# Performance work log

Measured on AMD Instinct MI355X. Metric: run time of the kernel, lower is better.

The kernel has to match this reference:

```python
import jax, jax.numpy as jnp
import numpy as np

DECAY = 0.8
EPS = 1e-05
COMMIT_W = 0.25
N, D, K = 32768, 128, 4096


def setup_inputs() -> dict:
    key = jax.random.key(0)
    k1, k2, k3, k4 = jax.random.split(key, 4)
    x = jax.random.normal(k1, (N, D), dtype=jnp.float32)
    embed = jax.random.normal(k2, (1, K, D), dtype=jnp.float32)
    cluster_size = jax.random.uniform(k3, (1, K), dtype=jnp.float32)
    embed_avg = jax.random.normal(k4, (1, K, D), dtype=jnp.float32)
    return {"x": x, "embed": embed, "cluster_size": cluster_size, "embed_avg": embed_avg}


def reference(x, embed, cluster_size, embed_avg):
    # x: [n, d]; embed: [1, K, d] (num_codebooks = 1, squeezed as in batched_embedding)
    e = embed[0]                                   # [K, d]
    K_ = e.shape[0]
    # negative squared euclidean distance (== -cdist^2 ordering, same argmin as -cdist)
    x2 = jnp.sum(x * x, axis=-1, keepdims=True)    # [n, 1]
    e2 = jnp.sum(e * e, axis=-1)                   # [K]
    dist = -(x2 - 2.0 * (x @ e.T) + e2)            # [n, K]
    embed_ind = jnp.argmax(dist, axis=-1)          # [n] cluster assignment (argmin distance)
    # differentiable embedding lookup (one-hot @ embed == gather)
    quantize = jnp.take(e, embed_ind, axis=0)      # [n, d]
    # EMA codebook statistics (training-time buffer updates)
    ones = jnp.ones((x.shape[0],), dtype=x.dtype)
    bins = jax.ops.segment_sum(ones, embed_ind, num_segments=K_)         # [K] bincount
    embed_sum = jax.ops.segment_sum(x, embed_ind, num_segments=K_)       # [K, d] scatter-add
    cs_new = cluster_size[0] * DECAY + (1.0 - DECAY) * bins
    ea_new = embed_avg[0] * DECAY + (1.0 - DECAY) * embed_sum
    n_total = jnp.sum(cs_new)
    cluster = (cs_new + EPS) / (n_total + K_ * EPS) * n_total            # laplace smoothing
    embed_normalized = ea_new / cluster[:, None]                         # [K, d]
    # commitment loss: mse(quantize.detach(), x) * weight
    commit_loss = COMMIT_W * jnp.mean((jax.lax.stop_gradient(quantize) - x) ** 2)
    return (quantize, embed_ind, commit_loss, cs_new[None], embed_normalized[None])
```

## Files before the change

kernel.cpp:

```cpp
#include <hip/hip_runtime.h>

#define NROWS 32768
#define DIM   128
#define KCODES 4096
#define DECAYF 0.8f
#define EPSF 1e-5f
#define COMMITW 0.25f

typedef _Float16 half8 __attribute__((ext_vector_type(8)));
typedef _Float16 half2v __attribute__((ext_vector_type(2)));
typedef float float4v __attribute__((ext_vector_type(4)));

__global__ __launch_bounds__(256) void esplit_kernel(const float* __restrict__ embed,
                                                     _Float16* __restrict__ estg,
                                                     float* __restrict__ e2h) {
    int code = blockIdx.x * 4 + (threadIdx.x >> 6);
    int lane = threadIdx.x & 63;
    float2 v = ((const float2*)(embed + (size_t)code * DIM))[lane];
    float s = v.x * v.x + v.y * v.y;
    #pragma unroll
    for (int off = 32; off > 0; off >>= 1) s += __shfl_down(s, off, 64);
    if (lane == 0) e2h[code] = 0.5f * s;

    int d = lane * 2;
    int ks = d >> 5, q = (d >> 3) & 3, j = d & 7;
    _Float16 h0 = (_Float16)v.x, l0 = (_Float16)(v.x - (float)h0);
    _Float16 h1 = (_Float16)v.y, l1 = (_Float16)(v.y - (float)h1);
    int chunk = code >> 6, c6 = code & 63;
    size_t base = (size_t)chunk * 16384;
    size_t hidx = base + (size_t)(( 0 + ks * 4 + q) * 64 + c6) * 8 + j;
    size_t lidx = base + (size_t)((16 + ks * 4 + q) * 64 + c6) * 8 + j;
    *(half2v*)&estg[hidx] = (half2v){h0, h1};
    *(half2v*)&estg[lidx] = (half2v){l0, l1};
}

__global__ __launch_bounds__(512, 2) void argmax_kernel(const float* __restrict__ x,
                                                        const _Float16* __restrict__ estg,
                                                        const float* __restrict__ e2h,
                                                        int* __restrict__ ind,
                                                        float* __restrict__ out_ind,
                                                        int* __restrict__ bins,
                                                        float* __restrict__ loss) {
    __shared__ float rv[8][64];
    __shared__ int   ri[8][64];
    __shared__ float x2s[128];

    int tid = threadIdx.x;
    int lane = tid & 63;
    int w = tid >> 6;
    int j = w & 3;
    int rh = w >> 2;
    int m15 = lane & 15;
    int q = (lane >> 4) & 3;
    int n0 = blockIdx.x * 128;

    half8 Ah[4][4], Al[4][4];
    float xsq[4];
    #pragma unroll
    for (int rt = 0; rt < 4; ++rt) {
        xsq[rt] = 0.f;
        #pragma unroll
        for (int ks = 0; ks < 4; ++ks) {
            const float* p = x + (size_t)(n0 + rh * 64 + rt * 16 + m15) * DIM + ks * 32 + q * 8;
            float4 a = *(const float4*)p;
            float4 b = *(const float4*)(p + 4);
            float f[8] = {a.x, a.y, a.z, a.w, b.x, b.y, b.z, b.w};
            half8 H, L;
            #pragma unroll
            for (int e = 0; e < 8; ++e) {
                _Float16 h = (_Float16)f[e];
                H[e] = h;
                L[e] = (_Float16)(f[e] - (float)h);
                xsq[rt] += f[e] * f[e];
            }
            Ah[rt][ks] = H;
            Al[rt][ks] = L;
        }
        xsq[rt] += __shfl_xor(xsq[rt], 16, 64);
        xsq[rt] += __shfl_xor(xsq[rt], 32, 64);
    }
    if (j == 0 && lane < 16) {
        #pragma unroll
        for (int rt = 0; rt < 4; ++rt) x2s[rh * 64 + rt * 16 + m15] = xsq[rt];
    }

    float best[4][4];
    int   bidx[4][4];
    #pragma unroll
    for (int rt = 0; rt < 4; ++rt)
        #pragma unroll
        for (int r = 0; r < 4; ++r) { best[rt][r] = -3.0e38f; bidx[rt][r] = 0; }

    const _Float16* bbase = estg + (size_t)(j * 16 + m15) * 8 + (size_t)q * 512;
    const int cm = j * 16 + m15;

    half8 B0h[4], B0l[4], B1h[4], B1l[4];
    float e20, e21;

    {
        const _Float16* cb = bbase;
        #pragma unroll
        for (int ks = 0; ks < 4; ++ks) {
            B0h[ks] = *(const half8*)(cb + ks * 2048);
            B0l[ks] = *(const half8*)(cb + 8192 + ks * 2048);
        }
        e20 = e2h[cm];
    }

    #pragma unroll 1
    for (int ch = 0; ch < 64; ch += 2) {
        {
            const _Float16* cb = bbase + (size_t)(ch + 1) * 16384;
            #pragma unroll
            for (int ks = 0; ks < 4; ++ks) {
                B1h[ks] = *(const half8*)(cb + ks * 2048);
                B1l[ks] = *(const half8*)(cb + 8192 + ks * 2048);
            }
            e21 = e2h[(ch + 1) * 64 + cm];
        }
        {
            float4v acc[4];
            #pragma unroll
            for (int rt = 0; rt < 4; ++rt) acc[rt] = (float4v){-e20, -e20, -e20, -e20};
            #pragma unroll
            for (int ks = 0; ks < 4; ++ks)
                #pragma unroll
                for (int rt = 0; rt < 4; ++rt) {
                    acc[rt] = __builtin_amdgcn_mfma_f32_16x16x32_f16(Ah[rt][ks], B0h[ks], acc[rt], 0, 0, 0);
                    acc[rt] = __builtin_amdgcn_mfma_f32_16x16x32_f16(Al[rt][ks], B0h[ks], acc[rt], 0, 0, 0);
                    acc[rt] = __builtin_amdgcn_mfma_f32_16x16x32_f16(Ah[rt][ks], B0l[ks], acc[rt], 0, 0, 0);
                }
            int c = ch * 64 + cm;
            #pragma unroll
            for (int rt = 0; rt < 4; ++rt)
                #pragma unroll
                for (int r = 0; r < 4; ++r) {
                    float s = acc[rt][r];
                    if (s > best[rt][r]) { best[rt][r] = s; bidx[rt][r] = c; }
                }
        }
        if (ch + 2 < 64) {
            const _Float16* cb = bbase + (size_t)(ch + 2) * 16384;
            #pragma unroll
            for (int ks = 0; ks < 4; ++ks) {
                B0h[ks] = *(const half8*)(cb + ks * 2048);
                B0l[ks] = *(const half8*)(cb + 8192 + ks * 2048);
            }
            e20 = e2h[(ch + 2) * 64 + cm];
        }
        {
            float4v acc[4];
            #pragma unroll
            for (int rt = 0; rt < 4; ++rt) acc[rt] = (float4v){-e21, -e21, -e21, -e21};
            #pragma unroll
            for (int ks = 0; ks < 4; ++ks)
                #pragma unroll
                for (int rt = 0; rt < 4; ++rt) {
                    acc[rt] = __builtin_amdgcn_mfma_f32_16x16x32_f16(Ah[rt][ks], B1h[ks], acc[rt], 0, 0, 0);
                    acc[rt] = __builtin_amdgcn_mfma_f32_16x16x32_f16(Al[rt][ks], B1h[ks], acc[rt], 0, 0, 0);
                    acc[rt] = __builtin_amdgcn_mfma_f32_16x16x32_f16(Ah[rt][ks], B1l[ks], acc[rt], 0, 0, 0);
                }
            int c = (ch + 1) * 64 + cm;
            #pragma unroll
            for (int rt = 0; rt < 4; ++rt)
                #pragma unroll
                for (int r = 0; r < 4; ++r) {
                    float s = acc[rt][r];
                    if (s > best[rt][r]) { best[rt][r] = s; bidx[rt][r] = c; }
                }
        }
    }

    #pragma unroll
    for (int rt = 0; rt < 4; ++rt)
        #pragma unroll
        for (int r = 0; r < 4; ++r) {
            float bv = best[rt][r];
            int   bi = bidx[rt][r];
            #pragma unroll
            for (int m = 1; m <= 8; m <<= 1) {
                float ov = __shfl_xor(bv, m, 64);
                int   oi = __shfl_xor(bi, m, 64);
                if (ov > bv || (ov == bv && oi < bi)) { bv = ov; bi = oi; }
            }
            if (m15 == 0) {
                int rl = rt * 16 + q * 4 + r;
                rv[w][rl] = bv;
                ri[w][rl] = bi;
            }
        }
    __syncthreads();
    if (tid < 128) {
        int rhh = tid >> 6;
        int rl  = tid & 63;
        float bv = rv[rhh * 4][rl];
        int   bi = ri[rhh * 4][rl];
        #pragma unroll
        for (int jj = 1; jj < 4; ++jj) {
            float ov = rv[rhh * 4 + jj][rl];
            int   oi = ri[rhh * 4 + jj][rl];
            if (ov > bv || (ov == bv && oi < bi)) { bv = ov; bi = oi; }
        }
        ind[n0 + tid] = bi;
        out_ind[n0 + tid] = (float)bi;
        atomicAdd(&bins[bi], 1);
        float lp = x2s[tid] - 2.0f * bv;
        #pragma unroll
        for (int off = 32; off > 0; off >>= 1) lp += __shfl_down(lp, off, 64);
        if ((tid & 63) == 0) atomicAdd(loss, lp);
    }
}

__global__ __launch_bounds__(1024) void scan_kernel(const int* __restrict__ bins,
                                                    const float* __restrict__ cluster_size,
                                                    const float* __restrict__ loss,
                                                    int* __restrict__ offsets,
                                                    int* __restrict__ cursor,
                                                    float* __restrict__ out_cs,
                                                    float* __restrict__ ntot,
                                                    float* __restrict__ out_loss) {
    __shared__ int   wtot[16];
    __shared__ float fred[16];
    int t = threadIdx.x;
    int lane = t & 63, wv = t >> 6;
    int b[4];
    float cs[4];
    float csum = 0.f;
    int s = 0;
    #pragma unroll
    for (int e = 0; e < 4; ++e) {
        b[e] = bins[t * 4 + e];
        s += b[e];
        cs[e] = cluster_size[t * 4 + e] * DECAYF + (1.0f - DECAYF) * (float)b[e];
        csum += cs[e];
    }
    int sc = s;
    #pragma unroll
    for (int off = 1; off < 64; off <<= 1) {
        int v = __shfl_up(sc, off, 64);
        if (lane >= off) sc += v;
    }
    float fc = csum;
    #pragma unroll
    for (int off = 32; off > 0; off >>= 1) fc += __shfl_down(fc, off, 64);
    if (lane == 63) wtot[wv] = sc;
    if (lane == 0) fred[wv] = fc;
    __syncthreads();
    if (t < 16) {
        int v = wtot[t];
        int scv = v;
        #pragma unroll
        for (int off = 1; off < 16; off <<= 1) {
            int u = __shfl_up(scv, off, 64);
            if (t >= off) scv += u;
        }
        wtot[t] = scv - v;
    }
    if (t == 0) {
        float tot = 0.f;
        #pragma unroll
        for (int i = 0; i < 16; ++i) tot += fred[i];
        *ntot = tot;
        *out_loss = COMMITW * (*loss) / (float)((size_t)NROWS * DIM);
    }
    __syncthreads();
    int ex = sc - s + wtot[wv];
    #pragma unroll
    for (int e = 0; e < 4; ++e) {
        offsets[t * 4 + e] = ex;
        cursor[t * 4 + e] = ex;
        out_cs[t * 4 + e] = cs[e];
        ex += b[e];
    }
}

__global__ __launch_bounds__(256) void reorder_kernel(const int* __restrict__ ind,
                                                      int* __restrict__ cursor,
                                                      int* __restrict__ rowids,
                                                      int* __restrict__ codesorted) {
    int row = blockIdx.x * 256 + threadIdx.x;
    int k = ind[row];
    int pos = atomicAdd(&cursor[k], 1);
    rowids[pos] = row;
    codesorted[pos] = k;
}

#define WROWS 16
__global__ __launch_bounds__(256) void segred_kernel(const float* __restrict__ x,
                                                     const float* __restrict__ embed,
                                                     const int* __restrict__ rowids,
                                                     const int* __restrict__ codesorted,
                                                     const int* __restrict__ offsets,
                                                     const int* __restrict__ bins,
                                                     float* __restrict__ esum,
                                                     float* __restrict__ out_q) {
    int tid = threadIdx.x;
    int lane = tid & 63;
    int wv = blockIdx.x * 4 + (tid >> 6);
    int w0 = wv * WROWS;

    int i16 = lane & (WROWS - 1);
    int rowv = rowids[w0 + i16];
    int kv   = codesorted[w0 + i16];

    float2 xv[WROWS];
    #pragma unroll
    for (int i = 0; i < WROWS; ++i) {
        int row = __shfl(rowv, i, 64);
        xv[i] = ((const float2*)(x + (size_t)row * DIM))[lane];
    }

    int curk = __shfl(kv, 0, 64);
    float2 qv = ((const float2*)(embed + (size_t)curk * DIM))[lane];
    float2 acc = {0.f, 0.f};

    #pragma unroll
    for (int i = 0; i < WROWS; ++i) {
        int row = __shfl(rowv, i, 64);
        int k   = __shfl(kv, i, 64);
        if (k != curk) {
            int sbeg = offsets[curk];
            int send = sbeg + bins[curk];
            float* ep = esum + (size_t)curk * DIM + lane * 2;
            if (sbeg >= w0 && send <= w0 + WROWS) {
                *(float2*)ep = acc;
            } else {
                atomicAdd(ep, acc.x);
                atomicAdd(ep + 1, acc.y);
            }
            curk = k;
            acc = (float2){0.f, 0.f};
            qv = ((const float2*)(embed + (size_t)curk * DIM))[lane];
        }
        acc.x += xv[i].x;
        acc.y += xv[i].y;
        ((float2*)(out_q + (size_t)row * DIM))[lane] = qv;
    }
    {
        int sbeg = offsets[curk];
        int send = sbeg + bins[curk];
        float* ep = esum + (size_t)curk * DIM + lane * 2;
        if (sbeg >= w0 && send <= w0 + WROWS) {
            *(float2*)ep = acc;
        } else {
            atomicAdd(ep, acc.x);
            atomicAdd(ep + 1, acc.y);
        }
    }
}

__global__ __launch_bounds__(256) void norm_kernel(const float* __restrict__ esum,
                                                   const float* __restrict__ embed_avg,
                                                   const float* __restrict__ out_cs,
                                                   const float* __restrict__ ntot,
                                                   float* __restrict__ out_norm) {
    int idx = blockIdx.x * 256 + threadIdx.x;
    int k = idx >> 6;
    float nt = *ntot;
    float cs = out_cs[k];
    float cluster = (cs + EPSF) / (nt + (float)KCODES * EPSF) * nt;
    float inv = 1.0f / cluster;
    float2 es = ((const float2*)esum)[idx];
    float2 ea = ((const float2*)embed_avg)[idx];
    float2 o;
    o.x = (ea.x * DECAYF + (1.0f - DECAYF) * es.x) * inv;
    o.y = (ea.y * DECAYF + (1.0f - DECAYF) * es.y) * inv;
    ((float2*)out_norm)[idx] = o;
}

extern "C" void kernel_launch(void* const* d_in, const int* in_sizes, int n_in,
                              void* d_out, int out_size, void* d_ws, size_t ws_size,
                              hipStream_t stream) {
    const float* x            = (const float*)d_in[0];
    const float* embed        = (const float*)d_in[1];
    const float* cluster_size = (const float*)d_in[2];
    const float* embed_avg    = (const float*)d_in[3];

    float* out      = (float*)d_out;
    float* out_q    = out;
    float* out_ind  = out + 4194304;
    float* out_loss = out_ind + 32768;
    float* out_cs   = out_loss + 1;
    float* out_norm = out_cs + 4096;

    char* ws = (char*)d_ws;
    _Float16* estg = (_Float16*)ws;
    float* e2h   = (float*)(ws + 2097152);
    int*   ind   = (int*)(ws + 2113536);
    int*   offsets = (int*)(ws + 2244608);
    int*   cursor  = (int*)(ws + 2260992);
    int*   rowids  = (int*)(ws + 2277376);
    int*   codesorted = (int*)(ws + 2408448);
    float* loss  = (float*)(ws + 2539520);
    float* ntot  = loss + 1;
    int*   bins  = (int*)(ws + 2539776);
    float* esum  = (float*)(ws + 2556160);

    hipMemsetAsync(ws + 2539520, 0, 256 + 16384 + 2097152, stream);

    esplit_kernel<<<KCODES / 4, 256, 0, stream>>>(embed, estg, e2h);
    argmax_kernel<<<NROWS / 128, 512, 0, stream>>>(x, estg, e2h, ind, out_ind,
                                                   bins, loss);
    scan_kernel<<<1, 1024, 0, stream>>>(bins, cluster_size, loss, offsets, cursor,
                                        out_cs, ntot, out_loss);
    reorder_kernel<<<NROWS / 256, 256, 0, stream>>>(ind, cursor, rowids, codesorted);
    segred_kernel<<<NROWS / WROWS / 4, 256, 0, stream>>>(x, embed, rowids, codesorted,
                                                         offsets, bins, esum, out_q);
    norm_kernel<<<KCODES * DIM / 2 / 256, 256, 0, stream>>>(esum, embed_avg, out_cs,
                                                            ntot, out_norm);
}
```

Before: 195.2 us.

## Double argmax block threads, halve rows per wave, stream codebook k-slices

The argmax kernel now runs 1024 threads per block (16 waves), and each wave owns 32 rows instead of 64. This halves the A-fragment and accumulator registers per wave. The codebook chunk is no longer loaded whole and double-buffered; each k-slice is fetched just ahead of its MFMAs, which lowers register pressure enough to allow launch bounds of 4 blocks. The aim is higher occupancy to hide global-load latency, at the cost of twice as many codebook loads per block, since each B fragment now feeds only 2 row tiles, and less prefetch distance.

Measured after the change: 203.0 us. 4.0% more time.

```diff
diff --git a/kernel.cpp b/kernel.cpp
--- a/kernel.cpp
+++ b/kernel.cpp
@@ -34,15 +34,15 @@
     *(half2v*)&estg[lidx] = (half2v){l0, l1};
 }
 
-__global__ __launch_bounds__(512, 2) void argmax_kernel(const float* __restrict__ x,
-                                                        const _Float16* __restrict__ estg,
-                                                        const float* __restrict__ e2h,
-                                                        int* __restrict__ ind,
-                                                        float* __restrict__ out_ind,
-                                                        int* __restrict__ bins,
-                                                        float* __restrict__ loss) {
-    __shared__ float rv[8][64];
-    __shared__ int   ri[8][64];
+__global__ __launch_bounds__(1024, 4) void argmax_kernel(const float* __restrict__ x,
+                                                         const _Float16* __restrict__ estg,
+                                                         const float* __restrict__ e2h,
+                                                         int* __restrict__ ind,
+                                                         float* __restrict__ out_ind,
+                                                         int* __restrict__ bins,
+                                                         float* __restrict__ loss) {
+    __shared__ float rv[16][32];
+    __shared__ int   ri[16][32];
     __shared__ float x2s[128];
 
     int tid = threadIdx.x;
@@ -54,14 +54,14 @@
     int q = (lane >> 4) & 3;
     int n0 = blockIdx.x * 128;
 
-    half8 Ah[4][4], Al[4][4];
-    float xsq[4];
-    #pragma unroll
-    for (int rt = 0; rt < 4; ++rt) {
+    half8 Ah[2][4], Al[2][4];
+    float xsq[2];
+    #pragma unroll
+    for (int rt = 0; rt < 2; ++rt) {
         xsq[rt] = 0.f;
         #pragma unroll
         for (int ks = 0; ks < 4; ++ks) {
-            const float* p = x + (size_t)(n0 + rh * 64 + rt * 16 + m15) * DIM + ks * 32 + q * 8;
+            const float* p = x + (size_t)(n0 + rh * 32 + rt * 16 + m15) * DIM + ks * 32 + q * 8;
             float4 a = *(const float4*)p;
             float4 b = *(const float4*)(p + 4);
             float f[8] = {a.x, a.y, a.z, a.w, b.x, b.y, b.z, b.w};
@@ -81,98 +81,80 @@
     }
     if (j == 0 && lane < 16) {
         #pragma unroll
-        for (int rt = 0; rt < 4; ++rt) x2s[rh * 64 + rt * 16 + m15] = xsq[rt];
-    }
-
-    float best[4][4];
-    int   bidx[4][4];
-    #pragma unroll
-    for (int rt = 0; rt < 4; ++rt)
+        for (int rt = 0; rt < 2; ++rt) x2s[rh * 32 + rt * 16 + m15] = xsq[rt];
+    }
+
+    float best[2][4];
+    int   bidx[2][4];
+    #pragma unroll
+    for (int rt = 0; rt < 2; ++rt)
         #pragma unroll
         for (int r = 0; r < 4; ++r) { best[rt][r] = -3.0e38f; bidx[rt][r] = 0; }
 
-    const _Float16* bbase = estg + (size_t)(j * 16 + m15) * 8 + (size_t)q * 512;
     const int cm = j * 16 + m15;
-
-    half8 B0h[4], B0l[4], B1h[4], B1l[4];
-    float e20, e21;
-
-    {
-        const _Float16* cb = bbase;
-        #pragma unroll
-        for (int ks = 0; ks < 4; ++ks) {
-            B0h[ks] = *(const half8*)(cb + ks * 2048);
-            B0l[ks] = *(const half8*)(cb + 8192 + ks * 2048);
-        }
-        e20 = e2h[cm];
-    }
+    const _Float16* cb = estg + (size_t)cm * 8 + (size_t)q * 512;
+
+    half8 BhA, BlA, BhB, BlB;
+    float e2cur, e2nxt;
+
+    BhA = *(const half8*)(cb);
+    BlA = *(const half8*)(cb + 8192);
+    e2cur = e2h[cm];
 
     #pragma unroll 1
-    for (int ch = 0; ch < 64; ch += 2) {
-        {
-            const _Float16* cb = bbase + (size_t)(ch + 1) * 16384;
+    for (int ch = 0; ch < 64; ++ch) {
+        float4v acc[2];
+        #pragma unroll
+        for (int rt = 0; rt < 2; ++rt) acc[rt] = (float4v){-e2cur, -e2cur, -e2cur, -e2cur};
+
+        BhB = *(const half8*)(cb + 2048);
+        BlB = *(const half8*)(cb + 8192 + 2048);
+        #pragma unroll
+        for (int rt = 0; rt < 2; ++rt) {
+            acc[rt] = __builtin_amdgcn_mfma_f32_16x16x32_f16(Ah[rt][0], BhA, acc[rt], 0, 0, 0);
+            acc[rt] = __builtin_amdgcn_mfma_f32_16x16x32_f16(Al[rt][0], BhA, acc[rt], 0, 0, 0);
+            acc[rt] = __builtin_amdgcn_mfma_f32_16x16x32_f16(Ah[rt][0], BlA, acc[rt], 0, 0, 0);
+        }
+        BhA = *(const half8*)(cb + 4096);
+        BlA = *(const half8*)(cb + 8192 + 4096);
+        #pragma unroll
+        for (int rt = 0; rt < 2; ++rt) {
+            acc[rt] = __builtin_amdgcn_mfma_f32_16x16x32_f16(Ah[rt][1], BhB, acc[rt], 0, 0, 0);
+            acc[rt] = __builtin_amdgcn_mfma_f32_16x16x32_f16(Al[rt][1], BhB, acc[rt], 0, 0, 0);
+            acc[rt] = __builtin_amdgcn_mfma_f32_16x16x32_f16(Ah[rt][1], BlB, acc[rt], 0, 0, 0);
+        }
+        BhB = *(const half8*)(cb + 6144);
+        BlB = *(const half8*)(cb + 8192 + 6144);
+        #pragma unroll
+        for (int rt = 0; rt < 2; ++rt) {
+            acc[rt] = __builtin_amdgcn_mfma_f32_16x16x32_f16(Ah[rt][2], BhA, acc[rt], 0, 0, 0);
+            acc[rt] = __builtin_amdgcn_mfma_f32_16x16x32_f16(Al[rt][2], BhA, acc[rt], 0, 0, 0);
+            acc[rt] = __builtin_amdgcn_mfma_f32_16x16x32_f16(Ah[rt][2], BlA, acc[rt], 0, 0, 0);
+        }
+        BhA = *(const half8*)(cb + 16384);
+        BlA = *(const half8*)(cb + 16384 + 8192);
+        e2nxt = e2h[(ch + 1) * 64 + cm];
+        #pragma unroll
+        for (int rt = 0; rt < 2; ++rt) {
+            acc[rt] = __builtin_amdgcn_mfma_f32_16x16x32_f16(Ah[rt][3], BhB, acc[rt], 0, 0, 0);
+            acc[rt] = __builtin_amdgcn_mfma_f32_16x16x32_f16(Al[rt][3], BhB, acc[rt], 0, 0, 0);
+            acc[rt] = __builtin_amdgcn_mfma_f32_16x16x32_f16(Ah[rt][3], BlB, acc[rt], 0, 0, 0);
+        }
+
+        int c = ch * 64 + cm;
+        #pragma unroll
+        for (int rt = 0; rt < 2; ++rt)
             #pragma unroll
-            for (int ks = 0; ks < 4; ++ks) {
-                B1h[ks] = *(const half8*)(cb + ks * 2048);
-                B1l[ks] = *(const half8*)(cb + 8192 + ks * 2048);
-            }
-            e21 = e2h[(ch + 1) * 64 + cm];
-        }
-        {
-            float4v acc[4];
-            #pragma unroll
-            for (int rt = 0; rt < 4; ++rt) acc[rt] = (float4v){-e20, -e20, -e20, -e20};
-            #pragma unroll
-            for (int ks = 0; ks < 4; ++ks)
-                #pragma unroll
-                for (int rt = 0; rt < 4; ++rt) {
-                    acc[rt] = __builtin_amdgcn_mfma_f32_16x16x32_f16(Ah[rt][ks], B0h[ks], acc[rt], 0, 0, 0);
-                    acc[rt] = __builtin_amdgcn_mfma_f32_16x16x32_f16(Al[rt][ks], B0h[ks], acc[rt], 0, 0, 0);
-                    acc[rt] = __builtin_amdgcn_mfma_f32_16x16x32_f16(Ah[rt][ks], B0l[ks], acc[rt], 0, 0, 0);
-                }
-            int c = ch * 64 + cm;
-            #pragma unroll
-            for (int rt = 0; rt < 4; ++rt)
-                #pragma unroll
-                for (int r = 0; r < 4; ++r) {
-                    float s = acc[rt][r];
-                    if (s > best[rt][r]) { best[rt][r] = s; bidx[rt][r] = c; }
-                }
-        }
-        if (ch + 2 < 64) {
-            const _Float16* cb = bbase + (size_t)(ch + 2) * 16384;
-            #pragma unroll
-            for (int ks = 0; ks < 4; ++ks) {
-                B0h[ks] = *(const half8*)(cb + ks * 2048);
-                B0l[ks] = *(const half8*)(cb + 8192 + ks * 2048);
-            }
-            e20 = e2h[(ch + 2) * 64 + cm];
-        }
-        {
-            float4v acc[4];
-            #pragma unroll
-            for (int rt = 0; rt < 4; ++rt) acc[rt] = (float4v){-e21, -e21, -e21, -e21};
-            #pragma unroll
-            for (int ks = 0; ks < 4; ++ks)
-                #pragma unroll
-                for (int rt = 0; rt < 4; ++rt) {
-                    acc[rt] = __builtin_amdgcn_mfma_f32_16x16x32_f16(Ah[rt][ks], B1h[ks], acc[rt], 0, 0, 0);
-                    acc[rt] = __builtin_amdgcn_mfma_f32_16x16x32_f16(Al[rt][ks], B1h[ks], acc[rt], 0, 0, 0);
-                    acc[rt] = __builtin_amdgcn_mfma_f32_16x16x32_f16(Ah[rt][ks], B1l[ks], acc[rt], 0, 0, 0);
-                }
-            int c = (ch + 1) * 64 + cm;
-            #pragma unroll
-            for (int rt = 0; rt < 4; ++rt)
-                #pragma unroll
-                for (int r = 0; r < 4; ++r) {
-                    float s = acc[rt][r];
-                    if (s > best[rt][r]) { best[rt][r] = s; bidx[rt][r] = c; }
-                }
-        }
-    }
-
-    #pragma unroll
-    for (int rt = 0; rt < 4; ++rt)
+            for (int r = 0; r < 4; ++r) {
+                float s = acc[rt][r];
+                if (s > best[rt][r]) { best[rt][r] = s; bidx[rt][r] = c; }
+            }
+        e2cur = e2nxt;
+        cb += 16384;
+    }
+
+    #pragma unroll
+    for (int rt = 0; rt < 2; ++rt)
         #pragma unroll
         for (int r = 0; r < 4; ++r) {
             float bv = best[rt][r];
@@ -191,14 +173,14 @@
         }
     __syncthreads();
     if (tid < 128) {
-        int rhh = tid >> 6;
-        int rl  = tid & 63;
-        float bv = rv[rhh * 4][rl];
-        int   bi = ri[rhh * 4][rl];
+        int rh2 = tid >> 5;
+        int rl  = tid & 31;
+        float bv = rv[rh2 * 4][rl];
+        int   bi = ri[rh2 * 4][rl];
         #pragma unroll
         for (int jj = 1; jj < 4; ++jj) {
-            float ov = rv[rhh * 4 + jj][rl];
-            int   oi = ri[rhh * 4 + jj][rl];
+            float ov = rv[rh2 * 4 + jj][rl];
+            int   oi = ri[rh2 * 4 + jj][rl];
             if (ov > bv || (ov == bv && oi < bi)) { bv = ov; bi = oi; }
         }
         ind[n0 + tid] = bi;
@@ -399,8 +381,8 @@
     hipMemsetAsync(ws + 2539520, 0, 256 + 16384 + 2097152, stream);
 
     esplit_kernel<<<KCODES / 4, 256, 0, stream>>>(embed, estg, e2h);
-    argmax_kernel<<<NROWS / 128, 512, 0, stream>>>(x, estg, e2h, ind, out_ind,
-                                                   bins, loss);
+    argmax_kernel<<<NROWS / 128, 1024, 0, stream>>>(x, estg, e2h, ind, out_ind,
+                                                    bins, loss);
     scan_kernel<<<1, 1024, 0, stream>>>(bins, cluster_size, loss, offsets, cursor,
                                         out_cs, ntot, out_loss);
     reorder_kernel<<<NROWS / 256, 256, 0, stream>>>(ind, cursor, rowids, codesorted);
```

## Stage codebook chunks into an LDS ring via global_load_lds in argmax

Applied to the files above, without the earlier changes.

The argmax kernel now streams each 64-code codebook chunk, including its packed half-norms, into a three-slot LDS ring using asynchronous global-to-LDS loads, two chunks ahead. Each step is guarded by vmcnt waits and a block barrier. Previously every wave pulled its B fragments straight from global memory into double-buffered registers, so waves sharing a column group fetched the same data twice. The staging layout is rearranged so each wave reads its fragments contiguously from LDS, and the e2 values are interleaved into each chunk. The cost is about 99KB of LDS per block, a barrier per chunk, and aliasing the esum workspace over the staging buffer, with its memset moved to after the argmax phase.

Measured after the change: 223.8 us. +14.6%, slower.

```diff
diff --git a/kernel.cpp b/kernel.cpp
--- a/kernel.cpp
+++ b/kernel.cpp
@@ -7,40 +7,56 @@
 #define EPSF 1e-5f
 #define COMMITW 0.25f
 
+#define CH_N 64
+#define CH_BYTES 33024
+#define ESTG_BYTES (CH_N * CH_BYTES)
+
 typedef _Float16 half8 __attribute__((ext_vector_type(8)));
 typedef _Float16 half2v __attribute__((ext_vector_type(2)));
 typedef float float4v __attribute__((ext_vector_type(4)));
 
+__device__ inline void stage1k(const char* gsrc, char* ldsdst) {
+    __builtin_amdgcn_global_load_lds(
+        (const __attribute__((address_space(1))) void*)gsrc,
+        (__attribute__((address_space(3))) void*)ldsdst, 16, 0, 0);
+}
+__device__ inline void stage256(const char* gsrc, char* ldsdst) {
+    __builtin_amdgcn_global_load_lds(
+        (const __attribute__((address_space(1))) void*)gsrc,
+        (__attribute__((address_space(3))) void*)ldsdst, 4, 0, 0);
+}
+
 __global__ __launch_bounds__(256) void esplit_kernel(const float* __restrict__ embed,
-                                                     _Float16* __restrict__ estg,
-                                                     float* __restrict__ e2h) {
+                                                     char* __restrict__ estg) {
     int code = blockIdx.x * 4 + (threadIdx.x >> 6);
     int lane = threadIdx.x & 63;
     float2 v = ((const float2*)(embed + (size_t)code * DIM))[lane];
     float s = v.x * v.x + v.y * v.y;
     #pragma unroll
     for (int off = 32; off > 0; off >>= 1) s += __shfl_down(s, off, 64);
-    if (lane == 0) e2h[code] = 0.5f * s;
+
+    int ch = code >> 6, c6 = code & 63;
+    int jj = c6 >> 4, m15c = c6 & 15;
+    char* cbase = estg + (size_t)ch * CH_BYTES;
+    if (lane == 0) *(float*)(cbase + 32768 + c6 * 4) = 0.5f * s;
 
     int d = lane * 2;
-    int ks = d >> 5, q = (d >> 3) & 3, j = d & 7;
+    int ks = d >> 5, q = (d >> 3) & 3, e = d & 7;
     _Float16 h0 = (_Float16)v.x, l0 = (_Float16)(v.x - (float)h0);
     _Float16 h1 = (_Float16)v.y, l1 = (_Float16)(v.y - (float)h1);
-    int chunk = code >> 6, c6 = code & 63;
-    size_t base = (size_t)chunk * 16384;
-    size_t hidx = base + (size_t)(( 0 + ks * 4 + q) * 64 + c6) * 8 + j;
-    size_t lidx = base + (size_t)((16 + ks * 4 + q) * 64 + c6) * 8 + j;
-    *(half2v*)&estg[hidx] = (half2v){h0, h1};
-    *(half2v*)&estg[lidx] = (half2v){l0, l1};
+    size_t fh = (size_t)((0 * 4 + ks) * 4 + jj) * 1024 + (size_t)(q * 16 + m15c) * 16 + e * 2;
+    size_t fl = (size_t)((1 * 4 + ks) * 4 + jj) * 1024 + (size_t)(q * 16 + m15c) * 16 + e * 2;
+    *(half2v*)(cbase + fh) = (half2v){h0, h1};
+    *(half2v*)(cbase + fl) = (half2v){l0, l1};
 }
 
 __global__ __launch_bounds__(512, 2) void argmax_kernel(const float* __restrict__ x,
-                                                        const _Float16* __restrict__ estg,
-                                                        const float* __restrict__ e2h,
+                                                        const char* __restrict__ estg,
                                                         int* __restrict__ ind,
                                                         float* __restrict__ out_ind,
                                                         int* __restrict__ bins,
                                                         float* __restrict__ loss) {
+    __shared__ __align__(16) char ring[3][CH_BYTES];
     __shared__ float rv[8][64];
     __shared__ int   ri[8][64];
     __shared__ float x2s[128];
@@ -84,6 +100,15 @@
         for (int rt = 0; rt < 4; ++rt) x2s[rh * 64 + rt * 16 + m15] = xsq[rt];
     }
 
+    #pragma unroll
+    for (int p = 0; p < 2; ++p) {
+        const char* g = estg + (size_t)p * CH_BYTES + (size_t)w * 4096 + (size_t)lane * 16;
+        char* d = &ring[p][w * 4096];
+        #pragma unroll
+        for (int i = 0; i < 4; ++i) stage1k(g + i * 1024, d + i * 1024);
+        stage256(estg + (size_t)p * CH_BYTES + 32768 + (size_t)lane * 4, &ring[p][32768]);
+    }
+
     float best[4][4];
     int   bidx[4][4];
     #pragma unroll
@@ -91,84 +116,51 @@
         #pragma unroll
         for (int r = 0; r < 4; ++r) { best[rt][r] = -3.0e38f; bidx[rt][r] = 0; }
 
-    const _Float16* bbase = estg + (size_t)(j * 16 + m15) * 8 + (size_t)q * 512;
     const int cm = j * 16 + m15;
 
-    half8 B0h[4], B0l[4], B1h[4], B1l[4];
-    float e20, e21;
-
-    {
-        const _Float16* cb = bbase;
+    #pragma unroll 1
+    for (int ch = 0; ch < CH_N; ++ch) {
+        if (ch + 1 == CH_N) asm volatile("s_waitcnt vmcnt(0)" ::: "memory");
+        else                asm volatile("s_waitcnt vmcnt(5)" ::: "memory");
+        __builtin_amdgcn_s_barrier();
+        asm volatile("" ::: "memory");
+
+        if (ch + 2 < CH_N) {
+            const char* g = estg + (size_t)(ch + 2) * CH_BYTES + (size_t)w * 4096 + (size_t)lane * 16;
+            char* d = &ring[(ch + 2) % 3][w * 4096];
+            #pragma unroll
+            for (int i = 0; i < 4; ++i) stage1k(g + i * 1024, d + i * 1024);
+            stage256(estg + (size_t)(ch + 2) * CH_BYTES + 32768 + (size_t)lane * 4,
+                     &ring[(ch + 2) % 3][32768]);
+        }
+
+        const char* buf = ring[ch % 3];
+        float e2 = *(const float*)(buf + 32768 + cm * 4);
+
+        float4v acc[4];
+        #pragma unroll
+        for (int rt = 0; rt < 4; ++rt) acc[rt] = (float4v){-e2, -e2, -e2, -e2};
+
         #pragma unroll
         for (int ks = 0; ks < 4; ++ks) {
-            B0h[ks] = *(const half8*)(cb + ks * 2048);
-            B0l[ks] = *(const half8*)(cb + 8192 + ks * 2048);
-        }
-        e20 = e2h[cm];
-    }
-
-    #pragma unroll 1
-    for (int ch = 0; ch < 64; ch += 2) {
-        {
-            const _Float16* cb = bbase + (size_t)(ch + 1) * 16384;
+            half8 Bh = *(const half8*)(buf + (size_t)((0 * 4 + ks) * 4 + j) * 1024 + (size_t)lane * 16);
+            half8 Bl = *(const half8*)(buf + (size_t)((1 * 4 + ks) * 4 + j) * 1024 + (size_t)lane * 16);
             #pragma unroll
-            for (int ks = 0; ks < 4; ++ks) {
-                B1h[ks] = *(const half8*)(cb + ks * 2048);
-                B1l[ks] = *(const half8*)(cb + 8192 + ks * 2048);
-            }
-            e21 = e2h[(ch + 1) * 64 + cm];
-        }
-        {
-            float4v acc[4];
+            for (int rt = 0; rt < 4; ++rt) {
+                acc[rt] = __builtin_amdgcn_mfma_f32_16x16x32_f16(Ah[rt][ks], Bh, acc[rt], 0, 0, 0);
+                acc[rt] = __builtin_amdgcn_mfma_f32_16x16x32_f16(Al[rt][ks], Bh, acc[rt], 0, 0, 0);
+                acc[rt] = __builtin_amdgcn_mfma_f32_16x16x32_f16(Ah[rt][ks], Bl, acc[rt], 0, 0, 0);
+            }
+        }
+
+        int c = ch * 64 + cm;
+        #pragma unroll
+        for (int rt = 0; rt < 4; ++rt)
             #pragma unroll
-            for (int rt = 0; rt < 4; ++rt) acc[rt] = (float4v){-e20, -e20, -e20, -e20};
-            #pragma unroll
-            for (int ks = 0; ks < 4; ++ks)
-                #pragma unroll
-                for (int rt = 0; rt < 4; ++rt) {
-                    acc[rt] = __builtin_amdgcn_mfma_f32_16x16x32_f16(Ah[rt][ks], B0h[ks], acc[rt], 0, 0, 0);
-                    acc[rt] = __builtin_amdgcn_mfma_f32_16x16x32_f16(Al[rt][ks], B0h[ks], acc[rt], 0, 0, 0);
-                    acc[rt] = __builtin_amdgcn_mfma_f32_16x16x32_f16(Ah[rt][ks], B0l[ks], acc[rt], 0, 0, 0);
-                }
-            int c = ch * 64 + cm;
-            #pragma unroll
-            for (int rt = 0; rt < 4; ++rt)
-                #pragma unroll
-                for (int r = 0; r < 4; ++r) {
-                    float s = acc[rt][r];
-                    if (s > best[rt][r]) { best[rt][r] = s; bidx[rt][r] = c; }
-                }
-        }
-        if (ch + 2 < 64) {
-            const _Float16* cb = bbase + (size_t)(ch + 2) * 16384;
-            #pragma unroll
-            for (int ks = 0; ks < 4; ++ks) {
-                B0h[ks] = *(const half8*)(cb + ks * 2048);
-                B0l[ks] = *(const half8*)(cb + 8192 + ks * 2048);
-            }
-            e20 = e2h[(ch + 2) * 64 + cm];
-        }
-        {
-            float4v acc[4];
-            #pragma unroll
-            for (int rt = 0; rt < 4; ++rt) acc[rt] = (float4v){-e21, -e21, -e21, -e21};
-            #pragma unroll
-            for (int ks = 0; ks < 4; ++ks)
-                #pragma unroll
-                for (int rt = 0; rt < 4; ++rt) {
-                    acc[rt] = __builtin_amdgcn_mfma_f32_16x16x32_f16(Ah[rt][ks], B1h[ks], acc[rt], 0, 0, 0);
-                    acc[rt] = __builtin_amdgcn_mfma_f32_16x16x32_f16(Al[rt][ks], B1h[ks], acc[rt], 0, 0, 0);
-                    acc[rt] = __builtin_amdgcn_mfma_f32_16x16x32_f16(Ah[rt][ks], B1l[ks], acc[rt], 0, 0, 0);
-                }
-            int c = (ch + 1) * 64 + cm;
-            #pragma unroll
-            for (int rt = 0; rt < 4; ++rt)
-                #pragma unroll
-                for (int r = 0; r < 4; ++r) {
-                    float s = acc[rt][r];
-                    if (s > best[rt][r]) { best[rt][r] = s; bidx[rt][r] = c; }
-                }
-        }
+            for (int r = 0; r < 4; ++r) {
+                float s = acc[rt][r];
+                if (s > best[rt][r]) { best[rt][r] = s; bidx[rt][r] = c; }
+            }
     }
 
     #pragma unroll
@@ -384,26 +376,26 @@
     float* out_norm = out_cs + 4096;
 
     char* ws = (char*)d_ws;
-    _Float16* estg = (_Float16*)ws;
-    float* e2h   = (float*)(ws + 2097152);
-    int*   ind   = (int*)(ws + 2113536);
+    char*  estg = ws;
+    float* esum = (float*)ws;
+    int*   ind  = (int*)(ws + 2113536);
     int*   offsets = (int*)(ws + 2244608);
     int*   cursor  = (int*)(ws + 2260992);
     int*   rowids  = (int*)(ws + 2277376);
     int*   codesorted = (int*)(ws + 2408448);
-    float* loss  = (float*)(ws + 2539520);
-    float* ntot  = loss + 1;
-    int*   bins  = (int*)(ws + 2539776);
-    float* esum  = (float*)(ws + 2556160);
-
-    hipMemsetAsync(ws + 2539520, 0, 256 + 16384 + 2097152, stream);
-
-    esplit_kernel<<<KCODES / 4, 256, 0, stream>>>(embed, estg, e2h);
-    argmax_kernel<<<NROWS / 128, 512, 0, stream>>>(x, estg, e2h, ind, out_ind,
+    float* loss = (float*)(ws + 2539520);
+    float* ntot = loss + 1;
+    int*   bins = (int*)(ws + 2539776);
+
+    hipMemsetAsync(ws + 2539520, 0, 256 + 16384, stream);
+
+    esplit_kernel<<<KCODES / 4, 256, 0, stream>>>(embed, estg);
+    argmax_kernel<<<NROWS / 128, 512, 0, stream>>>(x, estg, ind, out_ind,
                                                    bins, loss);
     scan_kernel<<<1, 1024, 0, stream>>>(bins, cluster_size, loss, offsets, cursor,
                                         out_cs, ntot, out_loss);
     reorder_kernel<<<NROWS / 256, 256, 0, stream>>>(ind, cursor, rowids, codesorted);
+    hipMemsetAsync(ws, 0, 2097152, stream);
     segred_kernel<<<NROWS / WROWS / 4, 256, 0, stream>>>(x, embed, rowids, codesorted,
                                                          offsets, bins, esum, out_q);
     norm_kernel<<<KCODES * DIM / 2 / 256, 256, 0, stream>>>(esum, embed_avg, out_cs,
```
